# Optimization experiments

Measured on AMD Instinct MI355X. Metric: run time of the kernel, lower is better.

## Reference

```python
import jax, jax.numpy as jnp
import numpy as np

B, T, E, H = 2, 4096, 1024, 16
D = E // H
EPS = 1e-6


def setup_inputs() -> dict:
    key = jax.random.key(0)
    ks = jax.random.split(key, 9)
    s = 1.0 / np.sqrt(E)
    return {
        "x": jax.random.normal(ks[0], (B, T, E), dtype=jnp.float32),
        "wq": jax.random.uniform(ks[1], (E, E), jnp.float32, -s, s),
        "bq": jax.random.uniform(ks[2], (E,), jnp.float32, -s, s),
        "wk": jax.random.uniform(ks[3], (E, E), jnp.float32, -s, s),
        "bk": jax.random.uniform(ks[4], (E,), jnp.float32, -s, s),
        "wv": jax.random.uniform(ks[5], (E, E), jnp.float32, -s, s),
        "bv": jax.random.uniform(ks[6], (E,), jnp.float32, -s, s),
        "wo": jax.random.uniform(ks[7], (E, E), jnp.float32, -s, s),
        "bo": jax.random.uniform(ks[8], (E,), jnp.float32, -s, s),
    }


def _feature_map(x):
    # elu(x) + 1
    return jnp.where(x > 0, x + 1.0, jnp.exp(x))


def reference(x, wq, bq, wk, bk, wv, bv, wo, bo):
    b, t, e = x.shape
    q = _feature_map(x @ wq + bq).reshape(b, t, H, D)
    k = _feature_map(x @ wk + bk).reshape(b, t, H, D)
    v = (x @ wv + bv).reshape(b, t, H, D)

    # time-major for the recurrence: [T, B, H, D]
    qT = jnp.moveaxis(q, 1, 0)
    kT = jnp.moveaxis(k, 1, 0)
    vT = jnp.moveaxis(v, 1, 0)

    S0 = jnp.zeros((b, H, D, D), dtype=x.dtype)  # running sum of k \otimes v
    z0 = jnp.zeros((b, H, D), dtype=x.dtype)     # running sum of k

    def step(carry, qkv):
        S, z = carry
        qt, kt, vt = qkv
        S = S + jnp.einsum('bhd,bhe->bhde', kt, vt)
        z = z + kt
        num = jnp.einsum('bhd,bhde->bhe', qt, S)
        den = jnp.einsum('bhd,bhd->bh', qt, z)[..., None] + EPS
        return (S, z), num / den

    _, outT = jax.lax.scan(step, (S0, z0), (qT, kT, vT))  # [T, B, H, D]
    out = jnp.moveaxis(outT, 0, 1).reshape(b, t, e)
    return out @ wo + bo
```

## Files before the change

kernel.cpp:

```cpp
#include <hip/hip_runtime.h>
#include <hip/hip_bf16.h>
#include <cstdint>
#include <cstddef>

#define B_   2
#define T_   4096
#define E_   1024
#define H_   16
#define D_   64
#define M_   (B_ * T_)
#define KDIM 1024
#define NDIM 1024
#define EPSC 1e-6f
#define CT   128
#define NC   (T_ / CT)

typedef __attribute__((ext_vector_type(8))) short bf16x8;
typedef __attribute__((ext_vector_type(4))) float f32x4;

__device__ __forceinline__ float bf2f(uint32_t u) {
    union { uint32_t u; float f; } x; x.u = u << 16; return x.f;
}
__device__ __forceinline__ unsigned short f2bf(float f) {
    union { float f; uint32_t u; } x; x.f = f;
    uint32_t r = x.u + 0x7fffu + ((x.u >> 16) & 1u);
    return (unsigned short)(r >> 16);
}
__device__ __forceinline__ void gload16(const void* g, void* l) {
    __builtin_amdgcn_global_load_lds(
        (const __attribute__((address_space(1))) void*)g,
        (__attribute__((address_space(3))) void*)l, 16, 0, 0);
}

__global__ __launch_bounds__(256) void conv_bf16(
    const float* __restrict__ in, unsigned short* __restrict__ out)
{
    const int i = blockIdx.x * 256 + threadIdx.x;
    const float4* p = (const float4*)in;
    float4 a = p[i * 2], b = p[i * 2 + 1];
    ushort4 o0 = make_ushort4(f2bf(a.x), f2bf(a.y), f2bf(a.z), f2bf(a.w));
    ushort4 o1 = make_ushort4(f2bf(b.x), f2bf(b.y), f2bf(b.z), f2bf(b.w));
    *(ushort4*)&out[(size_t)i * 8] = o0;
    *(ushort4*)&out[(size_t)i * 8 + 4] = o1;
}

__global__ __launch_bounds__(256) void transpose_w4(
    const float* __restrict__ w0, const float* __restrict__ w1,
    const float* __restrict__ w2, const float* __restrict__ w3,
    unsigned short* __restrict__ o0, unsigned short* __restrict__ o1,
    unsigned short* __restrict__ o2, unsigned short* __restrict__ o3)
{
    const float* src; unsigned short* dst;
    switch (blockIdx.z) {
        case 0: src = w0; dst = o0; break;
        case 1: src = w1; dst = o1; break;
        case 2: src = w2; dst = o2; break;
        default: src = w3; dst = o3; break;
    }
    __shared__ float tile[64][65];
    const int t = threadIdx.x, tx = t & 63, ty = t >> 6;
    const int r0 = blockIdx.y * 64, c0 = blockIdx.x * 64;
#pragma unroll
    for (int i = 0; i < 16; ++i)
        tile[ty + i * 4][tx] = src[(size_t)(r0 + ty + i * 4) * KDIM + c0 + tx];
    __syncthreads();
#pragma unroll
    for (int i = 0; i < 16; ++i)
        dst[(size_t)(c0 + ty + i * 4) * KDIM + r0 + tx] = f2bf(tile[tx][ty + i * 4]);
}

template <int MODE>
__global__ __launch_bounds__(256) void gemm_bf16(
    const unsigned short* __restrict__ A,
    const unsigned short* __restrict__ Bt,
    const float* __restrict__ bias,
    unsigned short* __restrict__ outb,
    unsigned short* __restrict__ outb2,
    float* __restrict__ outf)
{
    __shared__ unsigned short As[128 * 32];
    __shared__ unsigned short Bs[128 * 32];

    const int tid  = threadIdx.x;
    const int lane = tid & 63;
    const int wave = tid >> 6;
    const int wr = wave >> 1, wc = wave & 1;
    const int row0 = blockIdx.y * 128;
    const int col0 = blockIdx.x * 128;

    f32x4 acc[4][4] = {};

    const unsigned short* Ag = A  + (size_t)(row0 + (tid >> 2)) * KDIM + (tid & 3) * 8;
    const unsigned short* Bg = Bt + (size_t)(col0 + (tid >> 2)) * KDIM + (tid & 3) * 8;
    unsigned short* AsW = As + wave * 512;
    unsigned short* BsW = Bs + wave * 512;

    const int fr = lane & 15;
    const int fk = (lane >> 4) * 8;

    for (int k0 = 0; k0 < KDIM; k0 += 32) {
        gload16(Ag + k0,              AsW);
        gload16(Ag + 64 * KDIM + k0,  AsW + 2048);
        gload16(Bg + k0,              BsW);
        gload16(Bg + 64 * KDIM + k0,  BsW + 2048);
        __syncthreads();

        bf16x8 af[4], bfr[4];
#pragma unroll
        for (int m = 0; m < 4; ++m)
            af[m] = *(const bf16x8*)&As[(wr * 64 + m * 16 + fr) * 32 + fk];
#pragma unroll
        for (int n = 0; n < 4; ++n)
            bfr[n] = *(const bf16x8*)&Bs[(wc * 64 + n * 16 + fr) * 32 + fk];
#pragma unroll
        for (int m = 0; m < 4; ++m)
#pragma unroll
            for (int n = 0; n < 4; ++n)
                acc[m][n] = __builtin_amdgcn_mfma_f32_16x16x32_bf16(
                    af[m], bfr[n], acc[m][n], 0, 0, 0);
        __syncthreads();
    }

    const int fcol = lane & 15;
    const int frow = (lane >> 4) * 4;
#pragma unroll
    for (int m = 0; m < 4; ++m) {
#pragma unroll
        for (int n = 0; n < 4; ++n) {
            const int col = col0 + wc * 64 + n * 16 + fcol;
            const float bval = bias[col];
            const int rbase = row0 + wr * 64 + m * 16 + frow;
            float vv[4];
#pragma unroll
            for (int j = 0; j < 4; ++j) {
                float v = acc[m][n][j] + bval;
                if (MODE == 1 || MODE == 3) v = (v > 0.f) ? (v + 1.f) : __expf(v);
                vv[j] = v;
            }
            if (MODE == 2) {
#pragma unroll
                for (int j = 0; j < 4; ++j)
                    outf[(size_t)(rbase + j) * NDIM + col] = vv[j];
            } else {
                const int h = col >> 6;
                const int d = col & 63;
                if (MODE == 1 || MODE == 3) {
#pragma unroll
                    for (int j = 0; j < 4; ++j) {
                        const int row = rbase + j;
                        const int bb = row >> 12;
                        const int tt = row & (T_ - 1);
                        outb[((((size_t)bb * H_ + h) * T_) + tt) * D_ + d] = f2bf(vv[j]);
                    }
                }
                if (MODE == 0 || MODE == 3) {
                    const int bb = rbase >> 12;
                    const int tt = rbase & (T_ - 1);
                    ushort4 tp = make_ushort4(f2bf(vv[0]), f2bf(vv[1]),
                                              f2bf(vv[2]), f2bf(vv[3]));
                    *(ushort4*)&outb2[(((size_t)bb * H_ + h) * D_ + d) * T_ + tt] = tp;
                }
            }
        }
    }
}

__global__ __launch_bounds__(256) void chunk_sums_mfma(
    const unsigned short* __restrict__ Kt,
    const unsigned short* __restrict__ Vt,
    unsigned short* __restrict__ Sl,
    unsigned short* __restrict__ Zl)
{
    const int tid = threadIdx.x, lane = tid & 63, w = tid >> 6;
    const int lo = lane & 15, hi = lane >> 4;
    const int cid = blockIdx.x, bh = cid >> 5, c = cid & 31, t0 = c * CT;
    const unsigned short* kT = Kt + (size_t)bh * 64 * T_ + t0;
    const unsigned short* vT = Vt + (size_t)bh * 64 * T_ + t0;

    const bf16x8 ones8 = {0x3F80, 0x3F80, 0x3F80, 0x3F80,
                          0x3F80, 0x3F80, 0x3F80, 0x3F80};
    f32x4 acc[5] = {};
#pragma unroll
    for (int kt = 0; kt < 4; ++kt) {
        bf16x8 af = *(const bf16x8*)&kT[(size_t)(w * 16 + lo) * T_ + kt * 32 + hi * 8];
        bf16x8 bfr[5];
#pragma unroll
        for (int et = 0; et < 4; ++et)
            bfr[et] = *(const bf16x8*)&vT[(size_t)(et * 16 + lo) * T_ + kt * 32 + hi * 8];
        bfr[4] = ones8;
#pragma unroll
        for (int et = 0; et < 5; ++et)
            acc[et] = __builtin_amdgcn_mfma_f32_16x16x32_bf16(af, bfr[et], acc[et], 0, 0, 0);
    }
    unsigned short* sO = Sl + (size_t)cid * 4096;
    const int d0 = w * 16 + hi * 4;
#pragma unroll
    for (int et = 0; et < 4; ++et) {
        const int e = et * 16 + lo;
        ushort4 pk = make_ushort4(f2bf(acc[et][0]), f2bf(acc[et][1]),
                                  f2bf(acc[et][2]), f2bf(acc[et][3]));
        *(ushort4*)&sO[e * 64 + d0] = pk;
    }
    if (lo == 0) {
        ushort4 pk = make_ushort4(f2bf(acc[4][0]), f2bf(acc[4][1]),
                                  f2bf(acc[4][2]), f2bf(acc[4][3]));
        *(ushort4*)&Zl[(size_t)cid * 64 + d0] = pk;
    }
}

__global__ __launch_bounds__(256) void chunk_scan_bf(
    unsigned short* __restrict__ S, unsigned short* __restrict__ Z)
{
    const int bh = blockIdx.y;
    const int f0 = blockIdx.x * 512 + threadIdx.x * 2;
    float a0 = 0.f, a1 = 0.f;
    unsigned short* base = S + (size_t)bh * NC * 4096 + f0;
    for (int c = 0; c < NC; ++c) {
        uint32_t* p = (uint32_t*)(base + (size_t)c * 4096);
        uint32_t v = *p;
        float c0 = bf2f(v & 0xffffu), c1 = bf2f(v >> 16);
        *p = (uint32_t)f2bf(a0) | ((uint32_t)f2bf(a1) << 16);
        a0 += c0; a1 += c1;
    }
    if (blockIdx.x == 0 && threadIdx.x < 32) {
        float b0 = 0.f, b1 = 0.f;
        unsigned short* zb = Z + (size_t)bh * NC * 64 + threadIdx.x * 2;
        for (int c = 0; c < NC; ++c) {
            uint32_t* p = (uint32_t*)(zb + (size_t)c * 64);
            uint32_t v = *p;
            float c0 = bf2f(v & 0xffffu), c1 = bf2f(v >> 16);
            *p = (uint32_t)f2bf(b0) | ((uint32_t)f2bf(b1) << 16);
            b0 += c0; b1 += c1;
        }
    }
}

__global__ __launch_bounds__(256) void chunk_attn_mfma(
    const unsigned short* __restrict__ Qb,
    const unsigned short* __restrict__ Kb,
    const unsigned short* __restrict__ Vt,
    const unsigned short* __restrict__ SpT,
    const unsigned short* __restrict__ Zp,
    unsigned short* __restrict__ att)
{
    __shared__ unsigned short lds[128 * 128];

    const int tid = threadIdx.x;
    const int lane = tid & 63;
    const int w = tid >> 6;
    const int lo = lane & 15, hi = lane >> 4;
    const int cid = blockIdx.x;
    const int bh = cid >> 5, c = cid & 31;
    const int t0 = c * CT;

    const unsigned short* qB = Qb + ((size_t)bh * T_ + t0) * 64;
    const unsigned short* kB = Kb + ((size_t)bh * T_ + t0) * 64;
    const unsigned short* vB = Vt + (size_t)bh * 64 * T_ + t0;
    const unsigned short* sB = SpT + (size_t)cid * 4096;
    const unsigned short* zB = Zp + (size_t)cid * 64;

    bf16x8 ka[2][2];
#pragma unroll
    for (int si = 0; si < 2; ++si)
#pragma unroll
        for (int kt = 0; kt < 2; ++kt)
            ka[si][kt] = *(const bf16x8*)&kB[(w * 32 + si * 16 + lo) * 64 + kt * 32 + hi * 8];

    f32x4 pacc[2][8] = {};
#pragma unroll
    for (int ti = 0; ti < 8; ++ti) {
        if (ti >= 2 * w) {
#pragma unroll
            for (int kt = 0; kt < 2; ++kt) {
                bf16x8 qf = *(const bf16x8*)&qB[(ti * 16 + lo) * 64 + kt * 32 + hi * 8];
                pacc[0][ti] = __builtin_amdgcn_mfma_f32_16x16x32_bf16(
                    ka[0][kt], qf, pacc[0][ti], 0, 0, 0);
                if (ti >= 2 * w + 1)
                    pacc[1][ti] = __builtin_amdgcn_mfma_f32_16x16x32_bf16(
                        ka[1][kt], qf, pacc[1][ti], 0, 0, 0);
            }
        }
    }
#pragma unroll
    for (int ti = 0; ti < 8; ++ti) {
        if (ti >= 2 * w) {
            const int t = ti * 16 + lo;
#pragma unroll
            for (int si = 0; si < 2; ++si) {
                const int s0 = w * 32 + si * 16 + hi * 4;
                ushort4 pk;
                unsigned short* pe = (unsigned short*)&pk;
#pragma unroll
                for (int j = 0; j < 4; ++j)
                    pe[j] = (s0 + j <= t) ? f2bf(pacc[si][ti][j]) : (unsigned short)0;
                *(ushort4*)((char*)lds + t * 256 + ((s0 * 2) ^ ((t & 7) << 4))) = pk;
            }
        }
    }
    __syncthreads();

    const bf16x8 ones8 = {0x3F80, 0x3F80, 0x3F80, 0x3F80,
                          0x3F80, 0x3F80, 0x3F80, 0x3F80};
    f32x4 acc[2][5] = {};
#pragma unroll
    for (int kt = 0; kt < 6; ++kt) {
        const int skt = kt - 2;
        if (kt < 2 || skt <= w) {
            bf16x8 bfr[5];
            if (kt < 2) {
#pragma unroll
                for (int et = 0; et < 4; ++et)
                    bfr[et] = *(const bf16x8*)&sB[(et * 16 + lo) * 64 + kt * 32 + hi * 8];
                bfr[4] = *(const bf16x8*)&zB[kt * 32 + hi * 8];
            } else {
#pragma unroll
                for (int et = 0; et < 4; ++et)
                    bfr[et] = *(const bf16x8*)&vB[(size_t)(et * 16 + lo) * T_ + skt * 32 + hi * 8];
                bfr[4] = ones8;
            }
#pragma unroll
            for (int m = 0; m < 2; ++m) {
                const int t = w * 32 + m * 16 + lo;
                bf16x8 af;
                if (kt < 2)
                    af = *(const bf16x8*)&qB[t * 64 + kt * 32 + hi * 8];
                else
                    af = *(const bf16x8*)((char*)lds + t * 256 +
                         (((skt * 32 + hi * 8) * 2) ^ ((t & 7) << 4)));
#pragma unroll
                for (int et = 0; et < 5; ++et)
                    acc[m][et] = __builtin_amdgcn_mfma_f32_16x16x32_bf16(
                        af, bfr[et], acc[m][et], 0, 0, 0);
            }
        }
    }

    __syncthreads();
#pragma unroll
    for (int m = 0; m < 2; ++m) {
#pragma unroll
        for (int j = 0; j < 4; ++j) {
            const int t = w * 32 + m * 16 + hi * 4 + j;
            const float rden = 1.f / (acc[m][4][j] + EPSC);
#pragma unroll
            for (int et = 0; et < 4; ++et) {
                const int e = et * 16 + lo;
                *(unsigned short*)((char*)lds + t * 144 + e * 2) =
                    f2bf(acc[m][et][j] * rden);
            }
        }
    }
    __syncthreads();
    const int b = bh >> 4, h = bh & 15;
#pragma unroll
    for (int r = 0; r < 4; ++r) {
        const int vid = tid + r * 256;
        const int t = vid >> 3, eg = vid & 7;
        uint4 val = *(const uint4*)((const char*)lds + t * 144 + eg * 16);
        *(uint4*)&att[(size_t)(b * T_ + t0 + t) * E_ + h * 64 + eg * 8] = val;
    }
}

extern "C" void kernel_launch(void* const* d_in, const int* in_sizes, int n_in,
                              void* d_out, int out_size, void* d_ws, size_t ws_size,
                              hipStream_t stream)
{
    const float* x  = (const float*)d_in[0];
    const float* wq = (const float*)d_in[1];
    const float* bq = (const float*)d_in[2];
    const float* wk = (const float*)d_in[3];
    const float* bk = (const float*)d_in[4];
    const float* wv = (const float*)d_in[5];
    const float* bv = (const float*)d_in[6];
    const float* wo = (const float*)d_in[7];
    const float* bo = (const float*)d_in[8];
    float* out = (float*)d_out;

    char* ws = (char*)d_ws;
    unsigned short* qb  = (unsigned short*)(ws);
    unsigned short* kb  = (unsigned short*)(ws + (size_t)16 * 1024 * 1024);
    unsigned short* ktb = (unsigned short*)(ws + (size_t)32 * 1024 * 1024);
    unsigned short* vtb = (unsigned short*)(ws + (size_t)48 * 1024 * 1024);
    unsigned short* xb  = (unsigned short*)(ws + (size_t)64 * 1024 * 1024);
    unsigned short* attb = xb;
    unsigned short* Sl  = (unsigned short*)(ws + (size_t)80 * 1024 * 1024);
    unsigned short* Zl  = (unsigned short*)(ws + (size_t)88 * 1024 * 1024);
    unsigned short* wqT = (unsigned short*)(ws + (size_t)88 * 1024 * 1024 + 128 * 1024);
    unsigned short* wkT = wqT + (size_t)KDIM * NDIM;
    unsigned short* wvT = wkT + (size_t)KDIM * NDIM;
    unsigned short* woT = wvT + (size_t)KDIM * NDIM;

    conv_bf16<<<M_ * KDIM / (256 * 8), 256, 0, stream>>>(x, xb);
    transpose_w4<<<dim3(16, 16, 4), 256, 0, stream>>>(wq, wk, wv, wo,
                                                      wqT, wkT, wvT, woT);

    const dim3 gg(NDIM / 128, M_ / 128);
    gemm_bf16<1><<<gg, 256, 0, stream>>>(xb, wqT, bq, qb, nullptr, nullptr);
    gemm_bf16<3><<<gg, 256, 0, stream>>>(xb, wkT, bk, kb, ktb, nullptr);
    gemm_bf16<0><<<gg, 256, 0, stream>>>(xb, wvT, bv, nullptr, vtb, nullptr);

    chunk_sums_mfma<<<B_ * H_ * NC, 256, 0, stream>>>(ktb, vtb, Sl, Zl);
    chunk_scan_bf<<<dim3(8, B_ * H_), 256, 0, stream>>>(Sl, Zl);
    chunk_attn_mfma<<<B_ * H_ * NC, 256, 0, stream>>>(qb, kb, vtb, Sl, Zl, attb);

    gemm_bf16<2><<<gg, 256, 0, stream>>>(attb, woT, bo, nullptr, nullptr, out);
}
```

Measured before the change: 189.9 us.

## Fuse QKV projections into one 256x256-tiled triple-buffered GEMM with swizzled grid

Replaces the three separate Q/K/V GEMM launches with one kernel over a concatenated weight (wqT, wkT, wvT contiguous) using 256x256 tiles, 512 threads, a three-stage LDS pipeline with XOR-swizzled layout and split A/B staging interleaved with MFMA. Block indices are swizzled for L2 locality, in both the fused kernel and the output GEMM. This cuts launch count and re-reads of x, and should overlap global loads with compute better. It costs a large LDS footprint (96KB) and high register pressure from 8x4 accumulators, which may limit occupancy.

```diff
diff --git a/kernel.cpp b/kernel.cpp
--- a/kernel.cpp
+++ b/kernel.cpp
@@ -69,14 +69,159 @@
         dst[(size_t)(c0 + ty + i * 4) * KDIM + r0 + tx] = f2bf(tile[tx][ty + i * 4]);
 }
 
-template <int MODE>
-__global__ __launch_bounds__(256) void gemm_bf16(
+__global__ __launch_bounds__(512, 2) void gemm_qkv3(
+    const unsigned short* __restrict__ A,
+    const unsigned short* __restrict__ Wt,
+    const float* __restrict__ bq, const float* __restrict__ bk,
+    const float* __restrict__ bv,
+    unsigned short* __restrict__ qb,  unsigned short* __restrict__ kb,
+    unsigned short* __restrict__ ktb, unsigned short* __restrict__ vtb)
+{
+    __shared__ char lds[98304];
+
+    const int tid  = threadIdx.x;
+    const int lane = tid & 63;
+    const int w    = tid >> 6;
+    const int wm   = w >> 2;
+    const int wn   = w & 3;
+    const int lo   = lane & 15, hi = lane >> 4;
+
+    const int orig = blockIdx.x;
+    const int swz  = (orig & 7) * 48 + (orig >> 3);
+    const int bx = swz % 12;
+    const int by = swz / 12;
+    const int row0 = by * 256;
+    const int col0 = bx * 256;
+
+    const unsigned short* pa0; const unsigned short* pa1;
+    const unsigned short* pb0; const unsigned short* pb1;
+    {
+        int X, Y, r, ko;
+        X = tid * 16;           Y = X ^ (((X >> 9) & 1) << 5);
+        r = ((Y >> 10) << 4) + ((Y >> 6) & 15);  ko = (Y & 63) >> 1;
+        pa0 = A  + (size_t)(row0 + r) * KDIM + ko;
+        pb0 = Wt + (size_t)(col0 + r) * KDIM + ko;
+        X = (512 + tid) * 16;   Y = X ^ (((X >> 9) & 1) << 5);
+        r = ((Y >> 10) << 4) + ((Y >> 6) & 15);  ko = (Y & 63) >> 1;
+        pa1 = A  + (size_t)(row0 + r) * KDIM + ko;
+        pb1 = Wt + (size_t)(col0 + r) * KDIM + ko;
+    }
+    const int woff = w * 1024;
+
+    const int rdb = lo * 64 + hi * 16;
+    const int fragoff = rdb ^ (((rdb >> 9) & 1) << 5);
+
+#define LDSA(b) (lds + (b) * 16384)
+#define LDSB(b) (lds + 49152 + (b) * 16384)
+#define STAGE_A(t, b) { gload16(pa0 + (t) * 32, LDSA(b) + woff); \
+                        gload16(pa1 + (t) * 32, LDSA(b) + 8192 + woff); }
+#define STAGE_B(t, b) { gload16(pb0 + (t) * 32, LDSB(b) + woff); \
+                        gload16(pb1 + (t) * 32, LDSB(b) + 8192 + woff); }
+
+    f32x4 acc[8][4] = {};
+    const int NT = KDIM / 32;
+
+    STAGE_A(0, 0); STAGE_B(0, 0);
+    STAGE_A(1, 1); STAGE_B(1, 1);
+    asm volatile("s_waitcnt vmcnt(4)" ::: "memory");
+    __builtin_amdgcn_s_barrier();
+
+    for (int t = 0; t < NT; ++t) {
+        const int cb = t % 3;
+        const char* bufA = LDSA(cb);
+        const char* bufB = LDSB(cb);
+        const int nb = (t + 2) % 3;
+        const bool more = (t + 2 < NT);
+
+        if (more) STAGE_A(t + 2, nb);
+        bf16x8 bfr[4], af[4];
+#pragma unroll
+        for (int n = 0; n < 4; ++n)
+            bfr[n] = *(const bf16x8*)(bufB + (wn * 4 + n) * 1024 + fragoff);
+#pragma unroll
+        for (int m = 0; m < 4; ++m)
+            af[m] = *(const bf16x8*)(bufA + (wm * 8 + m) * 1024 + fragoff);
+        asm volatile("s_waitcnt lgkmcnt(0)" ::: "memory");
+        __builtin_amdgcn_sched_barrier(0);
+        __builtin_amdgcn_s_setprio(1);
+#pragma unroll
+        for (int m = 0; m < 4; ++m)
+#pragma unroll
+            for (int n = 0; n < 4; ++n)
+                acc[m][n] = __builtin_amdgcn_mfma_f32_16x16x32_bf16(
+                    af[m], bfr[n], acc[m][n], 0, 0, 0);
+        __builtin_amdgcn_s_setprio(0);
+
+        if (more) STAGE_B(t + 2, nb);
+        bf16x8 af2[4];
+#pragma unroll
+        for (int m = 0; m < 4; ++m)
+            af2[m] = *(const bf16x8*)(bufA + (wm * 8 + 4 + m) * 1024 + fragoff);
+        asm volatile("s_waitcnt lgkmcnt(0)" ::: "memory");
+        __builtin_amdgcn_sched_barrier(0);
+        __builtin_amdgcn_s_setprio(1);
+#pragma unroll
+        for (int m = 0; m < 4; ++m)
+#pragma unroll
+            for (int n = 0; n < 4; ++n)
+                acc[4 + m][n] = __builtin_amdgcn_mfma_f32_16x16x32_bf16(
+                    af2[m], bfr[n], acc[4 + m][n], 0, 0, 0);
+        __builtin_amdgcn_s_setprio(0);
+
+        if (more) asm volatile("s_waitcnt vmcnt(4)" ::: "memory");
+        else      asm volatile("s_waitcnt vmcnt(0)" ::: "memory");
+        __builtin_amdgcn_s_barrier();
+    }
+#undef STAGE_A
+#undef STAGE_B
+#undef LDSA
+#undef LDSB
+
+    const int matid = bx >> 2;
+    const int lcol0 = (bx & 3) * 256;
+    const float* bias = (matid == 0) ? bq : (matid == 1) ? bk : bv;
+    const int fcol = lane & 15, frow4 = (lane >> 4) * 4;
+#pragma unroll
+    for (int m = 0; m < 8; ++m) {
+#pragma unroll
+        for (int n = 0; n < 4; ++n) {
+            const int lcol = lcol0 + wn * 64 + n * 16 + fcol;
+            const float bval = bias[lcol];
+            const int rbase = row0 + wm * 128 + m * 16 + frow4;
+            const int h = lcol >> 6, d = lcol & 63;
+            const int bb = rbase >> 12;
+            const int tt = rbase & (T_ - 1);
+            float vv[4];
+#pragma unroll
+            for (int j = 0; j < 4; ++j) {
+                float v = acc[m][n][j] + bval;
+                if (matid <= 1) v = (v > 0.f) ? (v + 1.f) : __expf(v);
+                vv[j] = v;
+            }
+            if (matid == 0) {
+#pragma unroll
+                for (int j = 0; j < 4; ++j)
+                    qb[((((size_t)bb * H_ + h) * T_) + tt + j) * D_ + d] = f2bf(vv[j]);
+            } else if (matid == 1) {
+#pragma unroll
+                for (int j = 0; j < 4; ++j)
+                    kb[((((size_t)bb * H_ + h) * T_) + tt + j) * D_ + d] = f2bf(vv[j]);
+                ushort4 tp = make_ushort4(f2bf(vv[0]), f2bf(vv[1]),
+                                          f2bf(vv[2]), f2bf(vv[3]));
+                *(ushort4*)&ktb[(((size_t)bb * H_ + h) * D_ + d) * T_ + tt] = tp;
+            } else {
+                ushort4 tp = make_ushort4(f2bf(vv[0]), f2bf(vv[1]),
+                                          f2bf(vv[2]), f2bf(vv[3]));
+                *(ushort4*)&vtb[(((size_t)bb * H_ + h) * D_ + d) * T_ + tt] = tp;
+            }
+        }
+    }
+}
+
+__global__ __launch_bounds__(256) void gemm_out(
     const unsigned short* __restrict__ A,
     const unsigned short* __restrict__ Bt,
-    const float* __restrict__ bias,
-    unsigned short* __restrict__ outb,
-    unsigned short* __restrict__ outb2,
-    float* __restrict__ outf)
+    const float* __restrict__ bias, float* __restrict__ outf)
 {
     __shared__ unsigned short As[128 * 32];
     __shared__ unsigned short Bs[128 * 32];
@@ -85,8 +230,11 @@
     const int lane = tid & 63;
     const int wave = tid >> 6;
     const int wr = wave >> 1, wc = wave & 1;
-    const int row0 = blockIdx.y * 128;
-    const int col0 = blockIdx.x * 128;
+    const int orig = blockIdx.x;
+    const int swz  = (orig & 7) * 64 + (orig >> 3);
+    const int bx = swz & 7, by = swz >> 3;
+    const int row0 = by * 128;
+    const int col0 = bx * 128;
 
     f32x4 acc[4][4] = {};
 
@@ -130,37 +278,9 @@
             const int col = col0 + wc * 64 + n * 16 + fcol;
             const float bval = bias[col];
             const int rbase = row0 + wr * 64 + m * 16 + frow;
-            float vv[4];
-#pragma unroll
-            for (int j = 0; j < 4; ++j) {
-                float v = acc[m][n][j] + bval;
-                if (MODE == 1 || MODE == 3) v = (v > 0.f) ? (v + 1.f) : __expf(v);
-                vv[j] = v;
-            }
-            if (MODE == 2) {
-#pragma unroll
-                for (int j = 0; j < 4; ++j)
-                    outf[(size_t)(rbase + j) * NDIM + col] = vv[j];
-            } else {
-                const int h = col >> 6;
-                const int d = col & 63;
-                if (MODE == 1 || MODE == 3) {
-#pragma unroll
-                    for (int j = 0; j < 4; ++j) {
-                        const int row = rbase + j;
-                        const int bb = row >> 12;
-                        const int tt = row & (T_ - 1);
-                        outb[((((size_t)bb * H_ + h) * T_) + tt) * D_ + d] = f2bf(vv[j]);
-                    }
-                }
-                if (MODE == 0 || MODE == 3) {
-                    const int bb = rbase >> 12;
-                    const int tt = rbase & (T_ - 1);
-                    ushort4 tp = make_ushort4(f2bf(vv[0]), f2bf(vv[1]),
-                                              f2bf(vv[2]), f2bf(vv[3]));
-                    *(ushort4*)&outb2[(((size_t)bb * H_ + h) * D_ + d) * T_ + tt] = tp;
-                }
-            }
+#pragma unroll
+            for (int j = 0; j < 4; ++j)
+                outf[(size_t)(rbase + j) * NDIM + col] = acc[m][n][j] + bval;
         }
     }
 }
@@ -394,14 +514,11 @@
     transpose_w4<<<dim3(16, 16, 4), 256, 0, stream>>>(wq, wk, wv, wo,
                                                       wqT, wkT, wvT, woT);
 
-    const dim3 gg(NDIM / 128, M_ / 128);
-    gemm_bf16<1><<<gg, 256, 0, stream>>>(xb, wqT, bq, qb, nullptr, nullptr);
-    gemm_bf16<3><<<gg, 256, 0, stream>>>(xb, wkT, bk, kb, ktb, nullptr);
-    gemm_bf16<0><<<gg, 256, 0, stream>>>(xb, wvT, bv, nullptr, vtb, nullptr);
+    gemm_qkv3<<<384, 512, 0, stream>>>(xb, wqT, bq, bk, bv, qb, kb, ktb, vtb);
 
     chunk_sums_mfma<<<B_ * H_ * NC, 256, 0, stream>>>(ktb, vtb, Sl, Zl);
     chunk_scan_bf<<<dim3(8, B_ * H_), 256, 0, stream>>>(Sl, Zl);
     chunk_attn_mfma<<<B_ * H_ * NC, 256, 0, stream>>>(qb, kb, vtb, Sl, Zl, attb);
 
-    gemm_bf16<2><<<gg, 256, 0, stream>>>(attb, woT, bo, nullptr, nullptr, out);
-}
+    gemm_out<<<512, 256, 0, stream>>>(attb, woT, bo, out);
+}
```

Measured after the change: 171.1 us. 9.9% less time.

## Fuse Q/K/V projections into one pipelined 256x128 GEMM with LDS-staged epilogue

Applied to the files above, without the earlier changes.

Replaces three separate QKV GEMM launches with one kernel that treats wq/wk/wv transposes as a single 3072-column weight. It uses 256x128 tiles, double-buffered LDS with XOR swizzle, a BK of 64, explicit waitcnt pipelining and s_setprio around the MFMAs. The epilogue stages results in LDS so that the head-major and transposed stores are coalesced 16-byte writes. It also adds block-index swizzling to both GEMMs for L2 locality. The fused kernel relies on wqT/wkT/wvT being contiguous in the workspace, and its large LDS footprint may limit occupancy.

```diff
diff --git a/kernel.cpp b/kernel.cpp
--- a/kernel.cpp
+++ b/kernel.cpp
@@ -69,14 +69,161 @@
         dst[(size_t)(c0 + ty + i * 4) * KDIM + r0 + tx] = f2bf(tile[tx][ty + i * 4]);
 }
 
-template <int MODE>
-__global__ __launch_bounds__(256) void gemm_bf16(
+__global__ __launch_bounds__(512, 2) void gemm_qkv_p(
+    const unsigned short* __restrict__ A,
+    const unsigned short* __restrict__ Wt,
+    const float* __restrict__ bq, const float* __restrict__ bk,
+    const float* __restrict__ bv,
+    unsigned short* __restrict__ qb,  unsigned short* __restrict__ kb,
+    unsigned short* __restrict__ ktb, unsigned short* __restrict__ vtb)
+{
+    __shared__ char lds[98304];
+
+    const int tid  = threadIdx.x;
+    const int lane = tid & 63;
+    const int w    = tid >> 6;
+    const int wm   = w >> 1;
+    const int wn   = w & 1;
+    const int lo   = lane & 15, hi = lane >> 4;
+
+    const int orig = blockIdx.x;
+    const int swz  = (orig & 7) * 96 + (orig >> 3);
+    const int bx = swz % 24;
+    const int by = swz / 24;
+    const int row0 = by * 256;
+    const int col0 = bx * 128;
+
+    int sr, skE;
+    { int X = tid * 16; int Y = X ^ (((X >> 7) & 7) << 4);
+      sr = Y >> 7; skE = (Y & 127) >> 1; }
+    const unsigned short* pa = A  + (size_t)(row0 + sr) * KDIM + skE;
+    const unsigned short* pb = Wt + (size_t)(col0 + sr) * KDIM + skE;
+
+#define BUFA(p) (lds + (p) * 32768)
+#define BUFB(p) (lds + 65536 + (p) * 16384)
+#define STGA(t) { char* d_ = BUFA((t) & 1) + tid * 16;                        \
+    _Pragma("unroll") for (int ch = 0; ch < 4; ++ch)                          \
+        gload16(pa + (size_t)ch * 64 * KDIM + (t) * 64, d_ + ch * 8192); }
+#define STGB(t) { char* d_ = BUFB((t) & 1) + tid * 16;                        \
+    _Pragma("unroll") for (int ch = 0; ch < 2; ++ch)                          \
+        gload16(pb + (size_t)ch * 64 * KDIM + (t) * 64, d_ + ch * 8192); }
+
+    const int koff0 = (hi * 16)       ^ ((lane & 7) << 4);
+    const int koff1 = (64 + hi * 16)  ^ ((lane & 7) << 4);
+
+    f32x4 acc[4][4] = {};
+    const int NT = KDIM / 64;
+
+    STGA(0); STGB(0); STGA(1);
+    asm volatile("s_waitcnt vmcnt(4)" ::: "memory");
+    __builtin_amdgcn_s_barrier();
+
+#pragma unroll 2
+    for (int t = 0; t < NT; ++t) {
+        const char* bA = BUFA(t & 1);
+        const char* bB = BUFB(t & 1);
+
+        if (t + 1 < NT) STGB(t + 1);
+
+        bf16x8 af[4][2], bfr[4][2];
+#pragma unroll
+        for (int m = 0; m < 4; ++m) {
+            const char* p = bA + (wm * 64 + m * 16 + lo) * 128;
+            af[m][0] = *(const bf16x8*)(p + koff0);
+            af[m][1] = *(const bf16x8*)(p + koff1);
+        }
+#pragma unroll
+        for (int n = 0; n < 4; ++n) {
+            const char* p = bB + (wn * 64 + n * 16 + lo) * 128;
+            bfr[n][0] = *(const bf16x8*)(p + koff0);
+            bfr[n][1] = *(const bf16x8*)(p + koff1);
+        }
+        __builtin_amdgcn_s_setprio(1);
+#pragma unroll
+        for (int kk = 0; kk < 2; ++kk)
+#pragma unroll
+            for (int m = 0; m < 4; ++m)
+#pragma unroll
+                for (int n = 0; n < 4; ++n)
+                    acc[m][n] = __builtin_amdgcn_mfma_f32_16x16x32_bf16(
+                        af[m][kk], bfr[n][kk], acc[m][n], 0, 0, 0);
+        __builtin_amdgcn_s_setprio(0);
+
+        asm volatile("s_waitcnt lgkmcnt(0)" ::: "memory");
+        __builtin_amdgcn_s_barrier();
+
+        if (t + 2 < NT) {
+            STGA(t + 2);
+            asm volatile("s_waitcnt vmcnt(4)" ::: "memory");
+        } else {
+            asm volatile("s_waitcnt vmcnt(0)" ::: "memory");
+        }
+        __builtin_amdgcn_s_barrier();
+    }
+#undef STGA
+#undef STGB
+#undef BUFA
+#undef BUFB
+
+    unsigned short* ep = (unsigned short*)lds;
+    const int matid = bx >> 3;
+    const float* bias = (matid == 0) ? bq : (matid == 1) ? bk : bv;
+#pragma unroll
+    for (int n = 0; n < 4; ++n) {
+        const int lcol = wn * 64 + n * 16 + lo;
+        const float bval = bias[(bx & 7) * 128 + lcol];
+#pragma unroll
+        for (int m = 0; m < 4; ++m) {
+            const int lr0 = wm * 64 + m * 16 + hi * 4;
+#pragma unroll
+            for (int j = 0; j < 4; ++j) {
+                float v = acc[m][n][j] + bval;
+                if (matid <= 1) v = (v > 0.f) ? (v + 1.f) : __expf(v);
+                ep[(lr0 + j) * 136 + lcol] = f2bf(v);
+            }
+        }
+    }
+    __syncthreads();
+
+    const int b   = row0 >> 12;
+    const int tg0 = row0 & (T_ - 1);
+    const int h0  = (bx & 7) * 2;
+
+    if (matid <= 1) {
+        unsigned short* dst0 = (matid == 0) ? qb : kb;
+#pragma unroll
+        for (int it = 0; it < 8; ++it) {
+            const int vid = it * 512 + tid;
+            const int head = vid >> 11;
+            const int rem = vid & 2047;
+            const int tr = rem >> 3, c8 = rem & 7;
+            uint4 v = *(const uint4*)&ep[tr * 136 + head * 64 + c8 * 8];
+            *(uint4*)&dst0[((size_t)((b * H_ + h0 + head) * T_) + tg0 + tr) * D_
+                           + c8 * 8] = v;
+        }
+    }
+    if (matid >= 1) {
+        unsigned short* dstT = (matid == 1) ? ktb : vtb;
+#pragma unroll
+        for (int it = 0; it < 8; ++it) {
+            const int vid = it * 512 + tid;
+            const int head = vid >> 11;
+            const int rem = vid & 2047;
+            const int d = rem & 63, t8 = rem >> 6;
+            unsigned short vals[8];
+#pragma unroll
+            for (int i = 0; i < 8; ++i)
+                vals[i] = ep[(t8 * 8 + i) * 136 + head * 64 + d];
+            *(uint4*)&dstT[((size_t)((b * H_ + h0 + head) * D_) + d) * T_
+                           + tg0 + t8 * 8] = *(const uint4*)vals;
+        }
+    }
+}
+
+__global__ __launch_bounds__(256) void gemm_out(
     const unsigned short* __restrict__ A,
     const unsigned short* __restrict__ Bt,
-    const float* __restrict__ bias,
-    unsigned short* __restrict__ outb,
-    unsigned short* __restrict__ outb2,
-    float* __restrict__ outf)
+    const float* __restrict__ bias, float* __restrict__ outf)
 {
     __shared__ unsigned short As[128 * 32];
     __shared__ unsigned short Bs[128 * 32];
@@ -85,8 +232,11 @@
     const int lane = tid & 63;
     const int wave = tid >> 6;
     const int wr = wave >> 1, wc = wave & 1;
-    const int row0 = blockIdx.y * 128;
-    const int col0 = blockIdx.x * 128;
+    const int orig = blockIdx.x;
+    const int swz  = (orig & 7) * 64 + (orig >> 3);
+    const int bx = swz & 7, by = swz >> 3;
+    const int row0 = by * 128;
+    const int col0 = bx * 128;
 
     f32x4 acc[4][4] = {};
 
@@ -130,37 +280,9 @@
             const int col = col0 + wc * 64 + n * 16 + fcol;
             const float bval = bias[col];
             const int rbase = row0 + wr * 64 + m * 16 + frow;
-            float vv[4];
-#pragma unroll
-            for (int j = 0; j < 4; ++j) {
-                float v = acc[m][n][j] + bval;
-                if (MODE == 1 || MODE == 3) v = (v > 0.f) ? (v + 1.f) : __expf(v);
-                vv[j] = v;
-            }
-            if (MODE == 2) {
-#pragma unroll
-                for (int j = 0; j < 4; ++j)
-                    outf[(size_t)(rbase + j) * NDIM + col] = vv[j];
-            } else {
-                const int h = col >> 6;
-                const int d = col & 63;
-                if (MODE == 1 || MODE == 3) {
-#pragma unroll
-                    for (int j = 0; j < 4; ++j) {
-                        const int row = rbase + j;
-                        const int bb = row >> 12;
-                        const int tt = row & (T_ - 1);
-                        outb[((((size_t)bb * H_ + h) * T_) + tt) * D_ + d] = f2bf(vv[j]);
-                    }
-                }
-                if (MODE == 0 || MODE == 3) {
-                    const int bb = rbase >> 12;
-                    const int tt = rbase & (T_ - 1);
-                    ushort4 tp = make_ushort4(f2bf(vv[0]), f2bf(vv[1]),
-                                              f2bf(vv[2]), f2bf(vv[3]));
-                    *(ushort4*)&outb2[(((size_t)bb * H_ + h) * D_ + d) * T_ + tt] = tp;
-                }
-            }
+#pragma unroll
+            for (int j = 0; j < 4; ++j)
+                outf[(size_t)(rbase + j) * NDIM + col] = acc[m][n][j] + bval;
         }
     }
 }
@@ -394,14 +516,11 @@
     transpose_w4<<<dim3(16, 16, 4), 256, 0, stream>>>(wq, wk, wv, wo,
                                                       wqT, wkT, wvT, woT);
 
-    const dim3 gg(NDIM / 128, M_ / 128);
-    gemm_bf16<1><<<gg, 256, 0, stream>>>(xb, wqT, bq, qb, nullptr, nullptr);
-    gemm_bf16<3><<<gg, 256, 0, stream>>>(xb, wkT, bk, kb, ktb, nullptr);
-    gemm_bf16<0><<<gg, 256, 0, stream>>>(xb, wvT, bv, nullptr, vtb, nullptr);
+    gemm_qkv_p<<<768, 512, 0, stream>>>(xb, wqT, bq, bk, bv, qb, kb, ktb, vtb);
 
     chunk_sums_mfma<<<B_ * H_ * NC, 256, 0, stream>>>(ktb, vtb, Sl, Zl);
     chunk_scan_bf<<<dim3(8, B_ * H_), 256, 0, stream>>>(Sl, Zl);
     chunk_attn_mfma<<<B_ * H_ * NC, 256, 0, stream>>>(qb, kb, vtb, Sl, Zl, attb);
 
-    gemm_bf16<2><<<gg, 256, 0, stream>>>(attb, woT, bo, nullptr, nullptr, out);
-}
+    gemm_out<<<512, 256, 0, stream>>>(attb, woT, bo, out);
+}
```

Measured after the change: 167.9 us. -11.6%, faster.
